# Performance work log

Hardware: AMD Instinct MI355X
Metric: run time of the kernel (lower is better)

Reference implementation:

```python
import jax, jax.numpy as jnp
import numpy as np


def setup_inputs() -> dict:
    key = jax.random.key(0)
    k = jax.random.split(key, 6)
    B = 65536
    return {
        "x": jax.random.normal(k[0], (B, 784), dtype=jnp.float32),
        "conv_w": jax.random.normal(k[1], (3, 3), dtype=jnp.float32),
        "fc1_w": jax.random.normal(k[2], (128, 676), dtype=jnp.float32) * 0.04,
        "fc1_b": jax.random.normal(k[3], (128,), dtype=jnp.float32),
        "fc2_w": jax.random.normal(k[4], (10, 128), dtype=jnp.float32) * 0.09,
        "fc2_b": jax.random.normal(k[5], (10,), dtype=jnp.float32),
    }


def reference(x, conv_w, fc1_w, fc1_b, fc2_w, fc2_b):
    B = x.shape[0]
    img = x.reshape(B, 1, 28, 28)  # NCHW, single channel
    # Valid cross-correlation with a 3x3 kernel (matches the torch sum(region*weight) loop)
    kern = conv_w.reshape(1, 1, 3, 3)  # OIHW
    conv = jax.lax.conv_general_dilated(
        img, kern, window_strides=(1, 1), padding="VALID",
        dimension_numbers=("NCHW", "OIHW", "NCHW"))  # [B,1,26,26]
    h = conv.reshape(B, 26 * 26)
    h = jax.nn.relu(h @ fc1_w.T + fc1_b)  # [B,128]
    logits = h @ fc2_w.T + fc2_b  # [B,10]
    return logits
```

## Files before the change

### kernel.cpp

```cpp
#include <hip/hip_runtime.h>

typedef __bf16 bf16x8 __attribute__((ext_vector_type(8)));
typedef float  f32x4  __attribute__((ext_vector_type(4)));

#define KDIM    784
#define KSTEP   32
#define NSTEPS  25
#define NCOLS   128
#define NT      8
#define WAVES   4
#define ROWS_PER_WAVE 32
#define ROWS_PER_BLOCK (WAVES * ROWS_PER_WAVE)
#define STAGE_BYTES 16384
#define HSH_PAD 132

__global__ __launch_bounds__(256) void prep_weff(
    const float* __restrict__ conv_w,
    const float* __restrict__ fc1_w,
    __bf16* __restrict__ wfrag)
{
  int idx = blockIdx.x * 256 + threadIdx.x;
  if (idx >= NSTEPS * NT * 64) return;
  int lane = idx & 63;
  int n    = (idx >> 6) & (NT - 1);
  int s    = idx >> 9;
  int col  = n * 16 + (lane & 15);
  int kb   = s * KSTEP + (lane >> 4) * 8;
  bf16x8 o;
#pragma unroll
  for (int j = 0; j < 8; ++j) {
    int k = kb + j;
    float v = 0.f;
    if (k < KDIM) {
      int r = k / 28, c = k % 28;
#pragma unroll
      for (int u = 0; u < 3; ++u)
#pragma unroll
        for (int w = 0; w < 3; ++w) {
          int p = r - u, q = c - w;
          if (p >= 0 && p < 26 && q >= 0 && q < 26)
            v = fmaf(conv_w[u * 3 + w], fc1_w[col * 676 + p * 26 + q], v);
        }
    }
    o[j] = (__bf16)v;
  }
  reinterpret_cast<bf16x8*>(wfrag)[idx] = o;
}

__device__ __forceinline__ bf16x8 pack8(f32x4 lo, f32x4 hi) {
  bf16x8 r;
  r[0] = (__bf16)lo[0]; r[1] = (__bf16)lo[1];
  r[2] = (__bf16)lo[2]; r[3] = (__bf16)lo[3];
  r[4] = (__bf16)hi[0]; r[5] = (__bf16)hi[1];
  r[6] = (__bf16)hi[2]; r[7] = (__bf16)hi[3];
  return r;
}

__device__ __forceinline__ void split8(f32x4 a, f32x4 b, bf16x8& hi, bf16x8& lo) {
#pragma unroll
  for (int j = 0; j < 4; ++j) {
    __bf16 h = (__bf16)a[j]; hi[j] = h; lo[j] = (__bf16)(a[j] - (float)h);
  }
#pragma unroll
  for (int j = 0; j < 4; ++j) {
    __bf16 h = (__bf16)b[j]; hi[4 + j] = h; lo[4 + j] = (__bf16)(b[j] - (float)h);
  }
}

__device__ __forceinline__ void stage_issue(
    const __bf16* __restrict__ wfrag, unsigned char* dstbuf,
    int stage, int wave, int lane, int nchunks)
{
#pragma unroll
  for (int c = 0; c < 4; ++c) {
    int cw = wave * 4 + c;
    if (cw < nchunks) {
      const unsigned char* src =
          (const unsigned char*)wfrag + (size_t)stage * STAGE_BYTES + cw * 1024 + lane * 16;
      unsigned char* dst = dstbuf + cw * 1024 + lane * 16;
      __builtin_amdgcn_global_load_lds(
          (const __attribute__((address_space(1))) unsigned int*)src,
          (__attribute__((address_space(3))) unsigned int*)dst,
          16, 0, 0);
    }
  }
}

__global__ __launch_bounds__(256, 2) void fused_mlp(
    const float*  __restrict__ x,
    const __bf16* __restrict__ wfrag,
    const float*  __restrict__ fc1_b,
    const float*  __restrict__ fc2_w,
    const float*  __restrict__ fc2_b,
    float*        __restrict__ out)
{
  __shared__ __align__(16) unsigned char smem[WAVES * ROWS_PER_WAVE * HSH_PAD * 4];
  float (*hsh)[ROWS_PER_WAVE][HSH_PAD] =
      reinterpret_cast<float (*)[ROWS_PER_WAVE][HSH_PAD]>(smem);

  int tid  = threadIdx.x;
  int wave = tid >> 6, lane = tid & 63;
  int lrow = lane & 15;
  int lgrp = lane >> 4;
  long wrow0 = (long)blockIdx.x * ROWS_PER_BLOCK + wave * ROWS_PER_WAVE;

  const float* xr0 = x + (wrow0 + lrow) * KDIM;
  const float* xr1 = xr0 + 16 * KDIM;

  f32x4 acc[2][NT];
#pragma unroll
  for (int m = 0; m < 2; ++m)
#pragma unroll
    for (int n = 0; n < NT; ++n) acc[m][n] = (f32x4){0.f, 0.f, 0.f, 0.f};

  stage_issue(wfrag, smem, 0, wave, lane, 16);
  int cur = 0;
  for (int t = 0; t < 12; ++t) {
    __syncthreads();
    stage_issue(wfrag, smem + (cur ^ 1) * STAGE_BYTES, t + 1, wave, lane,
                (t < 11) ? 16 : 8);

    int k0 = (2 * t) * KSTEP + lgrp * 8;
    f32x4 l00 = *(const f32x4*)(xr0 + k0);
    f32x4 h00 = *(const f32x4*)(xr0 + k0 + 4);
    f32x4 l01 = *(const f32x4*)(xr1 + k0);
    f32x4 h01 = *(const f32x4*)(xr1 + k0 + 4);
    f32x4 l10 = *(const f32x4*)(xr0 + k0 + KSTEP);
    f32x4 h10 = *(const f32x4*)(xr0 + k0 + KSTEP + 4);
    f32x4 l11 = *(const f32x4*)(xr1 + k0 + KSTEP);
    f32x4 h11 = *(const f32x4*)(xr1 + k0 + KSTEP + 4);

    const bf16x8* bp = (const bf16x8*)(smem + cur * STAGE_BYTES) + lane;

    {
      bf16x8 a0 = pack8(l00, h00), a1 = pack8(l01, h01);
      bf16x8 bf[NT];
#pragma unroll
      for (int n = 0; n < NT; ++n) bf[n] = bp[n * 64];
#pragma unroll
      for (int n = 0; n < NT; ++n) {
        acc[0][n] = __builtin_amdgcn_mfma_f32_16x16x32_bf16(a0, bf[n], acc[0][n], 0, 0, 0);
        acc[1][n] = __builtin_amdgcn_mfma_f32_16x16x32_bf16(a1, bf[n], acc[1][n], 0, 0, 0);
      }
    }
    {
      bf16x8 a0 = pack8(l10, h10), a1 = pack8(l11, h11);
      bf16x8 bf[NT];
#pragma unroll
      for (int n = 0; n < NT; ++n) bf[n] = bp[512 + n * 64];
#pragma unroll
      for (int n = 0; n < NT; ++n) {
        acc[0][n] = __builtin_amdgcn_mfma_f32_16x16x32_bf16(a0, bf[n], acc[0][n], 0, 0, 0);
        acc[1][n] = __builtin_amdgcn_mfma_f32_16x16x32_bf16(a1, bf[n], acc[1][n], 0, 0, 0);
      }
    }
    cur ^= 1;
  }

  __syncthreads();
  {
    bf16x8 a0, a1;
    if (lgrp < 2) {
      int k = (NSTEPS - 1) * KSTEP + lgrp * 8;
      f32x4 lo0 = *(const f32x4*)(xr0 + k);
      f32x4 hi0 = *(const f32x4*)(xr0 + k + 4);
      f32x4 lo1 = *(const f32x4*)(xr1 + k);
      f32x4 hi1 = *(const f32x4*)(xr1 + k + 4);
      a0 = pack8(lo0, hi0);
      a1 = pack8(lo1, hi1);
    } else {
#pragma unroll
      for (int j = 0; j < 8; ++j) { a0[j] = (__bf16)0.f; a1[j] = (__bf16)0.f; }
    }
    const bf16x8* bp = (const bf16x8*)(smem + cur * STAGE_BYTES) + lane;
#pragma unroll
    for (int n = 0; n < NT; ++n) {
      bf16x8 b = bp[n * 64];
      acc[0][n] = __builtin_amdgcn_mfma_f32_16x16x32_bf16(a0, b, acc[0][n], 0, 0, 0);
      acc[1][n] = __builtin_amdgcn_mfma_f32_16x16x32_bf16(a1, b, acc[1][n], 0, 0, 0);
    }
  }
  __syncthreads();

#pragma unroll
  for (int m = 0; m < 2; ++m)
#pragma unroll
    for (int n = 0; n < NT; ++n) {
      int col = n * 16 + lrow;
      float bias = fc1_b[col];
#pragma unroll
      for (int ri = 0; ri < 4; ++ri) {
        int rl = m * 16 + lgrp * 4 + ri;
        float v = acc[m][n][ri] + bias;
        hsh[wave][rl][col] = fmaxf(v, 0.f);
      }
    }
  __syncthreads();

  int osafe = (lrow < 10) ? lrow : 9;
  bf16x8 whi[4], wlo[4];
#pragma unroll
  for (int s2 = 0; s2 < 4; ++s2) {
    f32x4 w0 = *(const f32x4*)(fc2_w + osafe * NCOLS + s2 * 32 + lgrp * 8);
    f32x4 w1 = *(const f32x4*)(fc2_w + osafe * NCOLS + s2 * 32 + lgrp * 8 + 4);
    if (lrow >= 10) { w0 = (f32x4){0.f,0.f,0.f,0.f}; w1 = (f32x4){0.f,0.f,0.f,0.f}; }
    split8(w0, w1, whi[s2], wlo[s2]);
  }
  float b2 = (lrow < 10) ? fc2_b[lrow] : 0.f;

#pragma unroll
  for (int m2 = 0; m2 < 2; ++m2) {
    f32x4 acc2 = (f32x4){0.f, 0.f, 0.f, 0.f};
    const float* hr = &hsh[wave][m2 * 16 + lrow][0];
#pragma unroll
    for (int s2 = 0; s2 < 4; ++s2) {
      f32x4 h0 = *(const f32x4*)(hr + s2 * 32 + lgrp * 8);
      f32x4 h1 = *(const f32x4*)(hr + s2 * 32 + lgrp * 8 + 4);
      bf16x8 ahi, alo; split8(h0, h1, ahi, alo);
      acc2 = __builtin_amdgcn_mfma_f32_16x16x32_bf16(ahi, whi[s2], acc2, 0, 0, 0);
      acc2 = __builtin_amdgcn_mfma_f32_16x16x32_bf16(ahi, wlo[s2], acc2, 0, 0, 0);
      acc2 = __builtin_amdgcn_mfma_f32_16x16x32_bf16(alo, whi[s2], acc2, 0, 0, 0);
    }
    if (lrow < 10) {
#pragma unroll
      for (int ri = 0; ri < 4; ++ri)
        out[(wrow0 + m2 * 16 + lgrp * 4 + ri) * 10 + lrow] = acc2[ri] + b2;
    }
  }
}

extern "C" void kernel_launch(void* const* d_in, const int* in_sizes, int n_in,
                              void* d_out, int out_size, void* d_ws, size_t ws_size,
                              hipStream_t stream) {
  const float* x      = (const float*)d_in[0];
  const float* conv_w = (const float*)d_in[1];
  const float* fc1_w  = (const float*)d_in[2];
  const float* fc1_b  = (const float*)d_in[3];
  const float* fc2_w  = (const float*)d_in[4];
  const float* fc2_b  = (const float*)d_in[5];
  float* outp = (float*)d_out;
  __bf16* wfrag = (__bf16*)d_ws;

  int Btotal = in_sizes[0] / KDIM;
  int prep_threads = NSTEPS * NT * 64;

  hipLaunchKernelGGL(prep_weff, dim3((prep_threads + 255) / 256), dim3(256), 0, stream,
                     conv_w, fc1_w, wfrag);
  hipLaunchKernelGGL(fused_mlp, dim3(Btotal / ROWS_PER_BLOCK), dim3(256), 0, stream,
                     x, wfrag, fc1_b, fc2_w, fc2_b, outp);
}
```

Measured before the change: 52.38 us.

## Prefetch next x tile into registers and raise occupancy via smaller epilogue LDS

Loads the next K-step's activation slice from global memory into registers while the current step's MFMAs run, so global-load latency overlaps with compute. Processes the fc1-to-fc2 epilogue in 16-row chunks per wave, roughly halving the shared-memory footprint, and raises launch bounds from 2 to 3 blocks per CU. The goal is more memory-level parallelism for a bandwidth-bound stream over x. The trade-off is higher register pressure from the prefetch buffer combined with a tighter per-thread register cap, which could cause spills.

After: 50.86 us. -2.9%, faster.

```diff
diff --git a/kernel.cpp b/kernel.cpp
--- a/kernel.cpp
+++ b/kernel.cpp
@@ -13,6 +13,7 @@
 #define ROWS_PER_BLOCK (WAVES * ROWS_PER_WAVE)
 #define STAGE_BYTES 16384
 #define HSH_PAD 132
+#define HCHUNK  16
 
 __global__ __launch_bounds__(256) void prep_weff(
     const float* __restrict__ conv_w,
@@ -86,7 +87,7 @@
   }
 }
 
-__global__ __launch_bounds__(256, 2) void fused_mlp(
+__global__ __launch_bounds__(256, 3) void fused_mlp(
     const float*  __restrict__ x,
     const __bf16* __restrict__ wfrag,
     const float*  __restrict__ fc1_b,
@@ -94,9 +95,9 @@
     const float*  __restrict__ fc2_b,
     float*        __restrict__ out)
 {
-  __shared__ __align__(16) unsigned char smem[WAVES * ROWS_PER_WAVE * HSH_PAD * 4];
-  float (*hsh)[ROWS_PER_WAVE][HSH_PAD] =
-      reinterpret_cast<float (*)[ROWS_PER_WAVE][HSH_PAD]>(smem);
+  __shared__ __align__(16) unsigned char smem[WAVES * HCHUNK * HSH_PAD * 4];
+  float (*hsh)[HCHUNK][HSH_PAD] =
+      reinterpret_cast<float (*)[HCHUNK][HSH_PAD]>(smem);
 
   int tid  = threadIdx.x;
   int wave = tid >> 6, lane = tid & 63;
@@ -113,45 +114,66 @@
 #pragma unroll
     for (int n = 0; n < NT; ++n) acc[m][n] = (f32x4){0.f, 0.f, 0.f, 0.f};
 
+  f32x4 xv[8];
+#define LOAD_STAGE(T)                                          \
+  {                                                            \
+    int k0 = (2 * (T)) * KSTEP + lgrp * 8;                     \
+    xv[0] = *(const f32x4*)(xr0 + k0);                         \
+    xv[1] = *(const f32x4*)(xr0 + k0 + 4);                     \
+    xv[2] = *(const f32x4*)(xr1 + k0);                         \
+    xv[3] = *(const f32x4*)(xr1 + k0 + 4);                     \
+    xv[4] = *(const f32x4*)(xr0 + k0 + KSTEP);                 \
+    xv[5] = *(const f32x4*)(xr0 + k0 + KSTEP + 4);             \
+    xv[6] = *(const f32x4*)(xr1 + k0 + KSTEP);                 \
+    xv[7] = *(const f32x4*)(xr1 + k0 + KSTEP + 4);             \
+  }
+
   stage_issue(wfrag, smem, 0, wave, lane, 16);
+  LOAD_STAGE(0);
   int cur = 0;
+
   for (int t = 0; t < 12; ++t) {
     __syncthreads();
     stage_issue(wfrag, smem + (cur ^ 1) * STAGE_BYTES, t + 1, wave, lane,
                 (t < 11) ? 16 : 8);
 
-    int k0 = (2 * t) * KSTEP + lgrp * 8;
-    f32x4 l00 = *(const f32x4*)(xr0 + k0);
-    f32x4 h00 = *(const f32x4*)(xr0 + k0 + 4);
-    f32x4 l01 = *(const f32x4*)(xr1 + k0);
-    f32x4 h01 = *(const f32x4*)(xr1 + k0 + 4);
-    f32x4 l10 = *(const f32x4*)(xr0 + k0 + KSTEP);
-    f32x4 h10 = *(const f32x4*)(xr0 + k0 + KSTEP + 4);
-    f32x4 l11 = *(const f32x4*)(xr1 + k0 + KSTEP);
-    f32x4 h11 = *(const f32x4*)(xr1 + k0 + KSTEP + 4);
+    bf16x8 a00 = pack8(xv[0], xv[1]), a01 = pack8(xv[2], xv[3]);
+    bf16x8 a10 = pack8(xv[4], xv[5]), a11 = pack8(xv[6], xv[7]);
+
+    if (t < 11) {
+      LOAD_STAGE(t + 1);
+    } else {
+      if (lgrp < 2) {
+        int k = (NSTEPS - 1) * KSTEP + lgrp * 8;
+        xv[0] = *(const f32x4*)(xr0 + k);
+        xv[1] = *(const f32x4*)(xr0 + k + 4);
+        xv[2] = *(const f32x4*)(xr1 + k);
+        xv[3] = *(const f32x4*)(xr1 + k + 4);
+      } else {
+        xv[0] = (f32x4){0.f,0.f,0.f,0.f}; xv[1] = (f32x4){0.f,0.f,0.f,0.f};
+        xv[2] = (f32x4){0.f,0.f,0.f,0.f}; xv[3] = (f32x4){0.f,0.f,0.f,0.f};
+      }
+    }
 
     const bf16x8* bp = (const bf16x8*)(smem + cur * STAGE_BYTES) + lane;
-
     {
-      bf16x8 a0 = pack8(l00, h00), a1 = pack8(l01, h01);
       bf16x8 bf[NT];
 #pragma unroll
       for (int n = 0; n < NT; ++n) bf[n] = bp[n * 64];
 #pragma unroll
       for (int n = 0; n < NT; ++n) {
-        acc[0][n] = __builtin_amdgcn_mfma_f32_16x16x32_bf16(a0, bf[n], acc[0][n], 0, 0, 0);
-        acc[1][n] = __builtin_amdgcn_mfma_f32_16x16x32_bf16(a1, bf[n], acc[1][n], 0, 0, 0);
+        acc[0][n] = __builtin_amdgcn_mfma_f32_16x16x32_bf16(a00, bf[n], acc[0][n], 0, 0, 0);
+        acc[1][n] = __builtin_amdgcn_mfma_f32_16x16x32_bf16(a01, bf[n], acc[1][n], 0, 0, 0);
       }
     }
     {
-      bf16x8 a0 = pack8(l10, h10), a1 = pack8(l11, h11);
       bf16x8 bf[NT];
 #pragma unroll
       for (int n = 0; n < NT; ++n) bf[n] = bp[512 + n * 64];
 #pragma unroll
       for (int n = 0; n < NT; ++n) {
-        acc[0][n] = __builtin_amdgcn_mfma_f32_16x16x32_bf16(a0, bf[n], acc[0][n], 0, 0, 0);
-        acc[1][n] = __builtin_amdgcn_mfma_f32_16x16x32_bf16(a1, bf[n], acc[1][n], 0, 0, 0);
+        acc[0][n] = __builtin_amdgcn_mfma_f32_16x16x32_bf16(a10, bf[n], acc[0][n], 0, 0, 0);
+        acc[1][n] = __builtin_amdgcn_mfma_f32_16x16x32_bf16(a11, bf[n], acc[1][n], 0, 0, 0);
       }
     }
     cur ^= 1;
@@ -159,19 +181,8 @@
 
   __syncthreads();
   {
-    bf16x8 a0, a1;
-    if (lgrp < 2) {
-      int k = (NSTEPS - 1) * KSTEP + lgrp * 8;
-      f32x4 lo0 = *(const f32x4*)(xr0 + k);
-      f32x4 hi0 = *(const f32x4*)(xr0 + k + 4);
-      f32x4 lo1 = *(const f32x4*)(xr1 + k);
-      f32x4 hi1 = *(const f32x4*)(xr1 + k + 4);
-      a0 = pack8(lo0, hi0);
-      a1 = pack8(lo1, hi1);
-    } else {
-#pragma unroll
-      for (int j = 0; j < 8; ++j) { a0[j] = (__bf16)0.f; a1[j] = (__bf16)0.f; }
-    }
+    bf16x8 a0 = pack8(xv[0], xv[1]);
+    bf16x8 a1 = pack8(xv[2], xv[3]);
     const bf16x8* bp = (const bf16x8*)(smem + cur * STAGE_BYTES) + lane;
 #pragma unroll
     for (int n = 0; n < NT; ++n) {
@@ -180,21 +191,6 @@
       acc[1][n] = __builtin_amdgcn_mfma_f32_16x16x32_bf16(a1, b, acc[1][n], 0, 0, 0);
     }
   }
-  __syncthreads();
-
-#pragma unroll
-  for (int m = 0; m < 2; ++m)
-#pragma unroll
-    for (int n = 0; n < NT; ++n) {
-      int col = n * 16 + lrow;
-      float bias = fc1_b[col];
-#pragma unroll
-      for (int ri = 0; ri < 4; ++ri) {
-        int rl = m * 16 + lgrp * 4 + ri;
-        float v = acc[m][n][ri] + bias;
-        hsh[wave][rl][col] = fmaxf(v, 0.f);
-      }
-    }
   __syncthreads();
 
   int osafe = (lrow < 10) ? lrow : 9;
@@ -207,11 +203,23 @@
     split8(w0, w1, whi[s2], wlo[s2]);
   }
   float b2 = (lrow < 10) ? fc2_b[lrow] : 0.f;
+  float bcol[NT];
+#pragma unroll
+  for (int n = 0; n < NT; ++n) bcol[n] = fc1_b[n * 16 + lrow];
 
 #pragma unroll
   for (int m2 = 0; m2 < 2; ++m2) {
+#pragma unroll
+    for (int n = 0; n < NT; ++n) {
+      int col = n * 16 + lrow;
+#pragma unroll
+      for (int ri = 0; ri < 4; ++ri) {
+        int rl = lgrp * 4 + ri;
+        hsh[wave][rl][col] = fmaxf(acc[m2][n][ri] + bcol[n], 0.f);
+      }
+    }
     f32x4 acc2 = (f32x4){0.f, 0.f, 0.f, 0.f};
-    const float* hr = &hsh[wave][m2 * 16 + lrow][0];
+    const float* hr = &hsh[wave][lrow][0];
 #pragma unroll
     for (int s2 = 0; s2 < 4; ++s2) {
       f32x4 h0 = *(const f32x4*)(hr + s2 * 32 + lgrp * 8);
```
